# Optimization experiments

Measured on AMD Instinct MI355X. Metric: run time of the kernel, lower is better.

## Reference

```python
import jax, jax.numpy as jnp
import numpy as np

N = 50000      # nodes
F = 128        # in_features
OUT = 128      # out_features
E = 600000     # edges per adjacency (avg degree 12)
J = 2
BN_EPS = 1e-5


def setup_inputs() -> dict:
    key = jax.random.key(0)
    ks = jax.random.split(key, 10)
    x = jax.random.normal(ks[0], (N, F), dtype=jnp.float32)
    rows0 = jax.random.randint(ks[1], (E,), 0, N, dtype=jnp.int32)
    cols0 = jax.random.randint(ks[2], (E,), 0, N, dtype=jnp.int32)
    vals0 = jax.random.uniform(ks[3], (E,), dtype=jnp.float32)
    rows1 = jax.random.randint(ks[4], (E,), 0, N, dtype=jnp.int32)
    cols1 = jax.random.randint(ks[5], (E,), 0, N, dtype=jnp.int32)
    vals1 = jax.random.uniform(ks[6], (E,), dtype=jnp.float32)
    # Linear(J*F, OUT) params, torch default init U(-1/sqrt(fan_in), 1/sqrt(fan_in))
    lim = 1.0 / np.sqrt(J * F)
    W_fc = jax.random.uniform(ks[7], (OUT, J * F), dtype=jnp.float32, minval=-lim, maxval=lim)
    b_fc = jax.random.uniform(ks[8], (OUT,), dtype=jnp.float32, minval=-lim, maxval=lim)
    gamma = jnp.ones((OUT,), dtype=jnp.float32)
    beta = jnp.zeros((OUT,), dtype=jnp.float32)
    return {"x": x, "rows0": rows0, "cols0": cols0, "vals0": vals0,
            "rows1": rows1, "cols1": cols1, "vals1": vals1,
            "W_fc": W_fc, "b_fc": b_fc, "gamma": gamma, "beta": beta}


def _spmm(rows, cols, vals, x):
    # sparse [N,N] @ dense [N,F]: gather source features, weight, scatter-add to rows
    msgs = vals[:, None] * x[cols]                      # [E, F]
    return jax.ops.segment_sum(msgs, rows, num_segments=x.shape[0])  # [N, F]


def reference(x, rows0, cols0, vals0, rows1, cols1, vals1, W_fc, b_fc, gamma, beta):
    h = jnp.concatenate([_spmm(rows0, cols0, vals0, x),
                         _spmm(rows1, cols1, vals1, x)], axis=1)  # [N, J*F]
    y = h @ W_fc.T + b_fc                                         # [N, OUT]
    # BatchNorm1d (training mode: batch stats, biased variance)
    mean = jnp.mean(y, axis=0)
    var = jnp.mean((y - mean) ** 2, axis=0)
    return (y - mean) * jax.lax.rsqrt(var + BN_EPS) * gamma + beta
```

## Files before the change

### kernel.cpp

```cpp
#include <hip/hip_runtime.h>

#define N_NODES 50000
#define F_IN 128
#define OUT_F 128
#define JF 256
#define EDGES 600000
#define BN_EPS 1e-5f
#define MAXDEG 48
#define NPART 8
#define PART_ROWS 6250
#define CHUNK_E 2048
#define NCHUNK 586

#define SCAT_B (NPART * NCHUNK)
#define CONVX_B 6250
#define CONVW_B 32
#define BUILD_B (SCAT_B + CONVX_B + CONVW_B)
#define ROWS_PB 32
#define FUSE_B 1563
#define NCOPY 16

typedef __attribute__((ext_vector_type(8))) short short8;
typedef __attribute__((ext_vector_type(4))) float floatx4;
typedef __attribute__((ext_vector_type(4))) unsigned short ushortx4;

static __device__ __forceinline__ unsigned short f2bf(float f) {
    unsigned int x = __float_as_uint(f);
    unsigned int r = (x + 0x7fffu + ((x >> 16) & 1u)) >> 16;
    return (unsigned short)r;
}
static __device__ __forceinline__ float bflo(unsigned int p) { return __uint_as_float(p << 16); }
static __device__ __forceinline__ float bfhi(unsigned int p) { return __uint_as_float(p & 0xffff0000u); }

__global__ __launch_bounds__(256) void build_kernel(
    const int* __restrict__ rows0, const int* __restrict__ cols0, const float* __restrict__ vals0,
    const int* __restrict__ rows1, const int* __restrict__ cols1, const float* __restrict__ vals1,
    int* __restrict__ cnt0, int* __restrict__ cnt1,
    unsigned int* __restrict__ pe0, unsigned int* __restrict__ pe1,
    const floatx4* __restrict__ x4, ushortx4* __restrict__ xb4,
    const floatx4* __restrict__ W4, ushortx4* __restrict__ Wb4)
{
    int bid = blockIdx.x;
    int tid = threadIdx.x;
    if (bid < SCAT_B) {
        unsigned part = (unsigned)(bid & (NPART - 1));
        int c0 = (bid >> 3) * CHUNK_E;

        bool pure0 = (c0 + CHUNK_E <= EDGES);
        bool pure1 = (c0 >= EDGES) && (c0 + CHUNK_E <= 2 * EDGES);
        if (pure0 || pure1) {
            const int*   rows = pure1 ? rows1 : rows0;
            const int*   cols = pure1 ? cols1 : cols0;
            const float* vals = pure1 ? vals1 : vals0;
            int*          cnt = pure1 ? cnt1 : cnt0;
            unsigned int*  pe = pure1 ? pe1 : pe0;
            int eb = pure1 ? c0 - EDGES : c0;
            #pragma unroll
            for (int g = 0; g < 2; ++g) {
                int e = eb + g * 1024 + tid * 4;
                int4 rv = *(const int4*)(rows + e);
                int rr[4] = {rv.x, rv.y, rv.z, rv.w};
                #pragma unroll
                for (int j = 0; j < 4; ++j) {
                    int r = rr[j];
                    if ((unsigned)r / (unsigned)PART_ROWS == part) {
                        int ee = e + j;
                        int c = cols[ee];
                        float v = vals[ee];
                        int p = atomicAdd(&cnt[r], 1);
                        if (p < MAXDEG)
                            pe[(size_t)r * MAXDEG + p] = ((unsigned int)c << 16) | f2bf(v);
                    }
                }
            }
        } else {
            for (int i = 0; i < CHUNK_E / 256; ++i) {
                int e = c0 + i * 256 + tid;
                if (e < 2 * EDGES) {
                    bool s1 = e >= EDGES;
                    int ee = s1 ? e - EDGES : e;
                    int r = s1 ? rows1[ee] : rows0[ee];
                    if ((unsigned)r / (unsigned)PART_ROWS == part) {
                        int c = s1 ? cols1[ee] : cols0[ee];
                        float v = s1 ? vals1[ee] : vals0[ee];
                        int* cnt = s1 ? cnt1 : cnt0;
                        unsigned int* pe = s1 ? pe1 : pe0;
                        int p = atomicAdd(&cnt[r], 1);
                        if (p < MAXDEG)
                            pe[(size_t)r * MAXDEG + p] = ((unsigned int)c << 16) | f2bf(v);
                    }
                }
            }
        }
    } else if (bid < SCAT_B + CONVX_B) {
        int i = (bid - SCAT_B) * 256 + tid;
        floatx4 v = __builtin_nontemporal_load(&x4[i]);
        ushortx4 o;
        o.x = f2bf(v.x); o.y = f2bf(v.y); o.z = f2bf(v.z); o.w = f2bf(v.w);
        __builtin_nontemporal_store(o, &xb4[i]);
    } else {
        int i = (bid - SCAT_B - CONVX_B) * 256 + tid;
        floatx4 v = W4[i];
        ushortx4 o;
        o.x = f2bf(v.x); o.y = f2bf(v.y); o.z = f2bf(v.z); o.w = f2bf(v.w);
        Wb4[i] = o;
    }
}

static __device__ __forceinline__ void rec_u(
    unsigned int q, int lane,
    const unsigned int* __restrict__ xb32, float& A0, float& A1)
{
    unsigned int xv = xb32[(q >> 16) * 64 + lane];
    float vv = __uint_as_float(q << 16);
    A0 += vv * bflo(xv);
    A1 += vv * bfhi(xv);
}
static __device__ __forceinline__ void rec_m(
    unsigned int q, bool on, int lane,
    const unsigned int* __restrict__ xb32, float& A0, float& A1)
{
    unsigned int idx = on ? (q >> 16) : 0u;
    float vv = on ? __uint_as_float(q << 16) : 0.0f;
    unsigned int xv = xb32[idx * 64 + lane];
    A0 += vv * bflo(xv);
    A1 += vv * bfhi(xv);
}

__global__ __launch_bounds__(256, 6) void gather_gemm(
    const unsigned int* __restrict__ xb32,
    const int* __restrict__ cnt0, const unsigned int* __restrict__ pe0,
    const int* __restrict__ cnt1, const unsigned int* __restrict__ pe1,
    const ushort* __restrict__ Wb, const float* __restrict__ bias,
    float* __restrict__ y, float* __restrict__ stats)
{
    __shared__ unsigned int hsu[ROWS_PB * 128];
    __shared__ uint4 recs[2][ROWS_PB][6];
    __shared__ int   lcnt[2][ROWS_PB];
    __shared__ float lstat[256];

    int tid = threadIdx.x;
    int lane = tid & 63;
    int w = tid >> 6;
    int wu = __builtin_amdgcn_readfirstlane(w);
    int row0 = blockIdx.x * ROWS_PB;

    lstat[tid] = 0.f;

    {
        int idx = tid;
        #pragma unroll
        for (int pass = 0; pass < 2; ++pass) {
            if (idx < 384) {
                int lr = idx / 12;
                int rem = idx - lr * 12;
                int side = rem >= 6;
                int g = rem - side * 6;
                int r = row0 + lr; if (r >= N_NODES) r = N_NODES - 1;
                const unsigned int* pe = side ? pe1 : pe0;
                recs[side][lr][g] = *(const uint4*)(pe + (size_t)r * MAXDEG + g * 4);
            }
            idx += 256;
        }
        if (tid < 64) {
            int side = tid >= ROWS_PB;
            int lr = tid & (ROWS_PB - 1);
            int r = row0 + lr;
            int d = 0;
            if (r < N_NODES) d = (side ? cnt1 : cnt0)[r];
            if (d > MAXDEG) d = MAXDEG;
            lcnt[side][lr] = d;
        }
    }
    __syncthreads();

    for (int rr = 0; rr < 8; ++rr) {
        int lr = wu * 8 + rr;
        int r = row0 + lr;
        int d0 = __builtin_amdgcn_readfirstlane(lcnt[0][lr]);
        int d1 = __builtin_amdgcn_readfirstlane(lcnt[1][lr]);

        float aL0 = 0.f, aL1 = 0.f, aR0 = 0.f, aR1 = 0.f;

        #pragma unroll
        for (int g = 0; g < 6; ++g) {
            if (g * 4 < d0) {
                uint4 q = recs[0][lr][g];
                rec_u(q.x, lane, xb32, aL0, aL1);
                rec_m(q.y, g * 4 + 1 < d0, lane, xb32, aL0, aL1);
                rec_m(q.z, g * 4 + 2 < d0, lane, xb32, aL0, aL1);
                rec_m(q.w, g * 4 + 3 < d0, lane, xb32, aL0, aL1);
            }
        }
        #pragma unroll
        for (int g = 0; g < 6; ++g) {
            if (g * 4 < d1) {
                uint4 q = recs[1][lr][g];
                rec_u(q.x, lane, xb32, aR0, aR1);
                rec_m(q.y, g * 4 + 1 < d1, lane, xb32, aR0, aR1);
                rec_m(q.z, g * 4 + 2 < d1, lane, xb32, aR0, aR1);
                rec_m(q.w, g * 4 + 3 < d1, lane, xb32, aR0, aR1);
            }
        }
        if (d0 > 24)
            for (int p = 24; p < d0; ++p)
                rec_u(pe0[(size_t)r * MAXDEG + p], lane, xb32, aL0, aL1);
        if (d1 > 24)
            for (int p = 24; p < d1; ++p)
                rec_u(pe1[(size_t)r * MAXDEG + p], lane, xb32, aR0, aR1);

        unsigned int sw = (unsigned int)((lr & 7) << 4);
        unsigned int offL = ((unsigned int)(lr * 512 + lane * 4)) ^ sw;
        unsigned int offR = ((unsigned int)(lr * 512 + 256 + lane * 4)) ^ sw;
        *(unsigned int*)((char*)hsu + offL) =
            (unsigned int)f2bf(aL0) | ((unsigned int)f2bf(aL1) << 16);
        *(unsigned int*)((char*)hsu + offR) =
            (unsigned int)f2bf(aR0) | ((unsigned int)f2bf(aR1) << 16);
    }
    __syncthreads();

    floatx4 acc[2][2];
    #pragma unroll
    for (int rt = 0; rt < 2; ++rt)
        #pragma unroll
        for (int c = 0; c < 2; ++c)
            acc[rt][c] = (floatx4){0.f, 0.f, 0.f, 0.f};

    int colb = lane & 15;
    int kg = lane >> 4;
    const char* hbase = (const char*)hsu;
    const ushort* wp = Wb + (size_t)(w * 32 + colb) * JF + kg * 8;

    #pragma unroll
    for (int k0 = 0; k0 < 8; ++k0) {
        #pragma unroll
        for (int rt = 0; rt < 2; ++rt) {
            int arow = rt * 16 + colb;
            unsigned int asw = (unsigned int)((arow & 7) << 4);
            unsigned int aoff = ((unsigned int)(arow * 512 + k0 * 64 + kg * 16)) ^ asw;
            short8 a = *(const short8*)(hbase + aoff);
            #pragma unroll
            for (int c = 0; c < 2; ++c) {
                short8 b = *(const short8*)(wp + c * 16 * JF + k0 * 32);
                acc[rt][c] = __builtin_amdgcn_mfma_f32_16x16x32_bf16(a, b, acc[rt][c], 0, 0, 0);
            }
        }
    }

    int rq = kg * 4;
    #pragma unroll
    for (int rt = 0; rt < 2; ++rt) {
        #pragma unroll
        for (int c = 0; c < 2; ++c) {
            int col = w * 32 + c * 16 + colb;
            float bv = bias[col];
            float s = 0.f, s2 = 0.f;
            #pragma unroll
            for (int q = 0; q < 4; ++q) {
                int row = row0 + rt * 16 + rq + q;
                if (row < N_NODES) {
                    float val = acc[rt][c][q] + bv;
                    y[(size_t)row * OUT_F + col] = val;
                    s += val; s2 += val * val;
                }
            }
            atomicAdd(&lstat[col], s);
            atomicAdd(&lstat[128 + col], s2);
        }
    }
    __syncthreads();
    float* sdst = stats + (size_t)(blockIdx.x & (NCOPY - 1)) * 256;
    atomicAdd(&sdst[tid], lstat[tid]);
}

__global__ void bn_prep(const float* __restrict__ stats,
                        const float* __restrict__ gamma,
                        const float* __restrict__ beta,
                        float* __restrict__ ss)
{
    int o = threadIdx.x;
    if (o >= OUT_F) return;
    float s = 0.f, s2 = 0.f;
    #pragma unroll
    for (int c = 0; c < NCOPY; ++c) {
        s  += stats[c * 256 + o];
        s2 += stats[c * 256 + 128 + o];
    }
    float inv_n = 1.0f / (float)N_NODES;
    float mean = s * inv_n;
    float var  = s2 * inv_n - mean * mean;
    float sc = rsqrtf(var + BN_EPS) * gamma[o];
    ss[o] = sc;
    ss[OUT_F + o] = beta[o] - mean * sc;
}

__global__ __launch_bounds__(256) void bn_apply(
    float* __restrict__ y, const float* __restrict__ ss)
{
    size_t i = (size_t)blockIdx.x * blockDim.x + threadIdx.x;
    size_t total = (size_t)N_NODES * OUT_F / 4;
    if (i >= total) return;

    int c4 = (int)(i & (OUT_F / 4 - 1));
    float4 v  = ((const float4*)y)[i];
    float4 sc = ((const float4*)ss)[c4];
    float4 sh = ((const float4*)(ss + OUT_F))[c4];
    v.x = v.x * sc.x + sh.x;
    v.y = v.y * sc.y + sh.y;
    v.z = v.z * sc.z + sh.z;
    v.w = v.w * sc.w + sh.w;
    ((float4*)y)[i] = v;
}

extern "C" void kernel_launch(void* const* d_in, const int* in_sizes, int n_in,
                              void* d_out, int out_size, void* d_ws, size_t ws_size,
                              hipStream_t stream)
{
    const float* x     = (const float*)d_in[0];
    const int*   rows0 = (const int*)  d_in[1];
    const int*   cols0 = (const int*)  d_in[2];
    const float* vals0 = (const float*)d_in[3];
    const int*   rows1 = (const int*)  d_in[4];
    const int*   cols1 = (const int*)  d_in[5];
    const float* vals1 = (const float*)d_in[6];
    const float* W     = (const float*)d_in[7];
    const float* b     = (const float*)d_in[8];
    const float* gamma = (const float*)d_in[9];
    const float* beta  = (const float*)d_in[10];

    float* y = (float*)d_out;

    ushort* xb = (ushort*)d_ws;
    ushort* Wb = xb + (size_t)N_NODES * F_IN;
    unsigned int* pe0 = (unsigned int*)(Wb + OUT_F * JF);
    unsigned int* pe1 = pe0 + (size_t)N_NODES * MAXDEG;
    int* cnt0 = (int*)(pe1 + (size_t)N_NODES * MAXDEG);
    int* cnt1 = cnt0 + N_NODES;
    float* stats = (float*)(cnt1 + N_NODES);
    float* ss    = stats + NCOPY * 256;

    hipMemsetAsync(cnt0, 0, (2 * (size_t)N_NODES + NCOPY * 256) * sizeof(int), stream);

    build_kernel<<<BUILD_B, 256, 0, stream>>>(
        rows0, cols0, vals0, rows1, cols1, vals1,
        cnt0, cnt1, pe0, pe1,
        (const floatx4*)x, (ushortx4*)xb, (const floatx4*)W, (ushortx4*)Wb);

    gather_gemm<<<FUSE_B, 256, 0, stream>>>(
        (const unsigned int*)xb, cnt0, pe0, cnt1, pe1, Wb, b, y, stats);

    bn_prep<<<1, 128, 0, stream>>>(stats, gamma, beta, ss);
    bn_apply<<<CONVX_B, 256, 0, stream>>>(y, ss);
}
```

Measured before the change: 168.3 us.

## Split fused gather-GEMM into separate gather and GEMM kernels via bf16 buffer

Splits the fused gather+GEMM kernel in two. A lighter gather kernel (no shared h tile, higher occupancy bound) writes the aggregated features as bf16 to a padded global buffer in an interleaved left/right layout. A separate GEMM kernel then stages 64 rows per block into swizzled LDS and computes all 128 output columns per wave. The weight conversion is permuted to match the interleaved K ordering. This is meant to decouple the latency-bound gather from the MFMA stage, at the cost of an extra global round trip of the h matrix and one more kernel launch.

```diff
diff --git a/kernel.cpp b/kernel.cpp
--- a/kernel.cpp
+++ b/kernel.cpp
@@ -17,7 +17,10 @@
 #define CONVW_B 32
 #define BUILD_B (SCAT_B + CONVX_B + CONVW_B)
 #define ROWS_PB 32
-#define FUSE_B 1563
+#define GATH_B 1563
+#define GROWS 64
+#define GEMM_B 782
+#define HPAD 50048
 #define NCOPY 16
 
 typedef __attribute__((ext_vector_type(8))) short short8;
@@ -38,7 +41,7 @@
     int* __restrict__ cnt0, int* __restrict__ cnt1,
     unsigned int* __restrict__ pe0, unsigned int* __restrict__ pe1,
     const floatx4* __restrict__ x4, ushortx4* __restrict__ xb4,
-    const floatx4* __restrict__ W4, ushortx4* __restrict__ Wb4)
+    const float* __restrict__ W, uint2* __restrict__ Wb2)
 {
     int bid = blockIdx.x;
     int tid = threadIdx.x;
@@ -100,10 +103,14 @@
         __builtin_nontemporal_store(o, &xb4[i]);
     } else {
         int i = (bid - SCAT_B - CONVX_B) * 256 + tid;
-        floatx4 v = W4[i];
-        ushortx4 o;
-        o.x = f2bf(v.x); o.y = f2bf(v.y); o.z = f2bf(v.z); o.w = f2bf(v.w);
-        Wb4[i] = o;
+        int col = i >> 6, l = i & 63;
+        const float* wr = W + (size_t)col * JF;
+        float a0 = wr[2 * l], a1 = wr[2 * l + 1];
+        float b0 = wr[128 + 2 * l], b1 = wr[128 + 2 * l + 1];
+        uint2 o;
+        o.x = (unsigned int)f2bf(a0) | ((unsigned int)f2bf(a1) << 16);
+        o.y = (unsigned int)f2bf(b0) | ((unsigned int)f2bf(b1) << 16);
+        Wb2[col * 64 + l] = o;
     }
 }
 
@@ -127,25 +134,20 @@
     A1 += vv * bfhi(xv);
 }
 
-__global__ __launch_bounds__(256, 6) void gather_gemm(
+__global__ __launch_bounds__(256, 8) void gather_kernel(
     const unsigned int* __restrict__ xb32,
     const int* __restrict__ cnt0, const unsigned int* __restrict__ pe0,
     const int* __restrict__ cnt1, const unsigned int* __restrict__ pe1,
-    const ushort* __restrict__ Wb, const float* __restrict__ bias,
-    float* __restrict__ y, float* __restrict__ stats)
-{
-    __shared__ unsigned int hsu[ROWS_PB * 128];
+    uint2* __restrict__ hb)
+{
     __shared__ uint4 recs[2][ROWS_PB][6];
     __shared__ int   lcnt[2][ROWS_PB];
-    __shared__ float lstat[256];
 
     int tid = threadIdx.x;
     int lane = tid & 63;
     int w = tid >> 6;
     int wu = __builtin_amdgcn_readfirstlane(w);
     int row0 = blockIdx.x * ROWS_PB;
-
-    lstat[tid] = 0.f;
 
     {
         int idx = tid;
@@ -209,64 +211,75 @@
             for (int p = 24; p < d1; ++p)
                 rec_u(pe1[(size_t)r * MAXDEG + p], lane, xb32, aR0, aR1);
 
-        unsigned int sw = (unsigned int)((lr & 7) << 4);
-        unsigned int offL = ((unsigned int)(lr * 512 + lane * 4)) ^ sw;
-        unsigned int offR = ((unsigned int)(lr * 512 + 256 + lane * 4)) ^ sw;
-        *(unsigned int*)((char*)hsu + offL) =
-            (unsigned int)f2bf(aL0) | ((unsigned int)f2bf(aL1) << 16);
-        *(unsigned int*)((char*)hsu + offR) =
-            (unsigned int)f2bf(aR0) | ((unsigned int)f2bf(aR1) << 16);
+        uint2 o;
+        o.x = (unsigned int)f2bf(aL0) | ((unsigned int)f2bf(aL1) << 16);
+        o.y = (unsigned int)f2bf(aR0) | ((unsigned int)f2bf(aR1) << 16);
+        hb[(size_t)(row0 + lr) * 64 + lane] = o;
+    }
+}
+
+__global__ __launch_bounds__(256, 4) void gemm_kernel(
+    const uint4* __restrict__ hb4,
+    const ushort* __restrict__ Wb,
+    const float* __restrict__ bias,
+    float* __restrict__ y, float* __restrict__ stats)
+{
+    __shared__ char hsu[GROWS * 512];
+    __shared__ float lstat[256];
+
+    int tid = threadIdx.x;
+    int lane = tid & 63;
+    int w = tid >> 6;
+    int row0 = blockIdx.x * GROWS;
+
+    lstat[tid] = 0.f;
+
+    const char* src = (const char*)hb4 + (size_t)row0 * 512;
+    #pragma unroll
+    for (int u = tid; u < GROWS * 32; u += 256) {
+        int off = u * 16;
+        int row = off >> 9;
+        int dst = off ^ ((row & 7) << 4);
+        *(uint4*)(hsu + dst) = *(const uint4*)(src + off);
     }
     __syncthreads();
 
-    floatx4 acc[2][2];
-    #pragma unroll
-    for (int rt = 0; rt < 2; ++rt)
-        #pragma unroll
-        for (int c = 0; c < 2; ++c)
-            acc[rt][c] = (floatx4){0.f, 0.f, 0.f, 0.f};
+    floatx4 acc[8];
+    #pragma unroll
+    for (int c = 0; c < 8; ++c) acc[c] = (floatx4){0.f, 0.f, 0.f, 0.f};
 
     int colb = lane & 15;
     int kg = lane >> 4;
-    const char* hbase = (const char*)hsu;
-    const ushort* wp = Wb + (size_t)(w * 32 + colb) * JF + kg * 8;
+    int arow = w * 16 + colb;
+    unsigned int asw = (unsigned int)((arow & 7) << 4);
 
     #pragma unroll
     for (int k0 = 0; k0 < 8; ++k0) {
-        #pragma unroll
-        for (int rt = 0; rt < 2; ++rt) {
-            int arow = rt * 16 + colb;
-            unsigned int asw = (unsigned int)((arow & 7) << 4);
-            unsigned int aoff = ((unsigned int)(arow * 512 + k0 * 64 + kg * 16)) ^ asw;
-            short8 a = *(const short8*)(hbase + aoff);
-            #pragma unroll
-            for (int c = 0; c < 2; ++c) {
-                short8 b = *(const short8*)(wp + c * 16 * JF + k0 * 32);
-                acc[rt][c] = __builtin_amdgcn_mfma_f32_16x16x32_bf16(a, b, acc[rt][c], 0, 0, 0);
-            }
+        short8 a = *(const short8*)(hsu + (((unsigned int)(arow * 512 + k0 * 64 + kg * 16)) ^ asw));
+        #pragma unroll
+        for (int c = 0; c < 8; ++c) {
+            short8 b = *(const short8*)(Wb + (size_t)(c * 16 + colb) * 256 + k0 * 32 + kg * 8);
+            acc[c] = __builtin_amdgcn_mfma_f32_16x16x32_bf16(a, b, acc[c], 0, 0, 0);
         }
     }
 
     int rq = kg * 4;
     #pragma unroll
-    for (int rt = 0; rt < 2; ++rt) {
-        #pragma unroll
-        for (int c = 0; c < 2; ++c) {
-            int col = w * 32 + c * 16 + colb;
-            float bv = bias[col];
-            float s = 0.f, s2 = 0.f;
-            #pragma unroll
-            for (int q = 0; q < 4; ++q) {
-                int row = row0 + rt * 16 + rq + q;
-                if (row < N_NODES) {
-                    float val = acc[rt][c][q] + bv;
-                    y[(size_t)row * OUT_F + col] = val;
-                    s += val; s2 += val * val;
-                }
-            }
-            atomicAdd(&lstat[col], s);
-            atomicAdd(&lstat[128 + col], s2);
-        }
+    for (int c = 0; c < 8; ++c) {
+        int col = c * 16 + colb;
+        float bv = bias[col];
+        float s = 0.f, s2 = 0.f;
+        #pragma unroll
+        for (int q = 0; q < 4; ++q) {
+            int row = row0 + w * 16 + rq + q;
+            if (row < N_NODES) {
+                float val = acc[c][q] + bv;
+                y[(size_t)row * OUT_F + col] = val;
+                s += val; s2 += val * val;
+            }
+        }
+        atomicAdd(&lstat[col], s);
+        atomicAdd(&lstat[128 + col], s2);
     }
     __syncthreads();
     float* sdst = stats + (size_t)(blockIdx.x & (NCOPY - 1)) * 256;
@@ -334,7 +347,8 @@
     ushort* Wb = xb + (size_t)N_NODES * F_IN;
     unsigned int* pe0 = (unsigned int*)(Wb + OUT_F * JF);
     unsigned int* pe1 = pe0 + (size_t)N_NODES * MAXDEG;
-    int* cnt0 = (int*)(pe1 + (size_t)N_NODES * MAXDEG);
+    uint2* hb = (uint2*)(pe1 + (size_t)N_NODES * MAXDEG);
+    int* cnt0 = (int*)(hb + (size_t)HPAD * 64);
     int* cnt1 = cnt0 + N_NODES;
     float* stats = (float*)(cnt1 + N_NODES);
     float* ss    = stats + NCOPY * 256;
@@ -344,10 +358,13 @@
     build_kernel<<<BUILD_B, 256, 0, stream>>>(
         rows0, cols0, vals0, rows1, cols1, vals1,
         cnt0, cnt1, pe0, pe1,
-        (const floatx4*)x, (ushortx4*)xb, (const floatx4*)W, (ushortx4*)Wb);
-
-    gather_gemm<<<FUSE_B, 256, 0, stream>>>(
-        (const unsigned int*)xb, cnt0, pe0, cnt1, pe1, Wb, b, y, stats);
+        (const floatx4*)x, (ushortx4*)xb, W, (uint2*)Wb);
+
+    gather_kernel<<<GATH_B, 256, 0, stream>>>(
+        (const unsigned int*)xb, cnt0, pe0, cnt1, pe1, hb);
+
+    gemm_kernel<<<GEMM_B, 256, 0, stream>>>(
+        (const uint4*)hb, Wb, b, y, stats);
 
     bn_prep<<<1, 128, 0, stream>>>(stats, gamma, beta, ss);
     bn_apply<<<CONVX_B, 256, 0, stream>>>(y, ss);
```

Result: slower. 182.1 us (+8.2%).
